# Performance work log

Measured on AMD Instinct MI355X. Metric: run time of the kernel, lower is better.

The kernel has to match this reference:

```python
import jax, jax.numpy as jnp
import numpy as np

B, V, N, IN_F, HEADS, OUT_F = 4, 4, 1000, 64, 4, 32
D = HEADS * OUT_F  # 128, concat=True
E = 64000
NEG_SLOPE = 0.2


def setup_inputs() -> dict:
    key = jax.random.key(0)
    ks = jax.random.split(key, 8)
    x = jax.random.normal(ks[0], (B, V, N, IN_F), jnp.float32)
    edge_index = jax.random.randint(ks[1], (2, E), 0, B * N, dtype=jnp.int64)
    W = jax.random.normal(ks[2], (HEADS * OUT_F, IN_F), jnp.float32) / np.sqrt(IN_F)
    att = jax.random.normal(ks[3], (1, HEADS, 2 * OUT_F), jnp.float32) * 0.1
    in_proj_w = jax.random.normal(ks[4], (3 * D, D), jnp.float32) / np.sqrt(D)
    in_proj_b = jnp.zeros((3 * D,), jnp.float32)
    out_proj_w = jax.random.normal(ks[5], (D, D), jnp.float32) / np.sqrt(D)
    out_proj_b = jnp.zeros((D,), jnp.float32)
    bias = jnp.zeros((D,), jnp.float32)
    return dict(x=x, W=W, att=att, in_proj_w=in_proj_w, in_proj_b=in_proj_b,
                out_proj_w=out_proj_w, out_proj_b=out_proj_b, bias=bias,
                edge_index=edge_index)


def reference(x, W, att, in_proj_w, in_proj_b, out_proj_w, out_proj_b, bias, edge_index):
    Bx, Vx, Nx, _ = x.shape
    Ntot = Bx * Nx
    # intra-view GAT: shared W across views
    h = jnp.einsum('bvni,oi->bvno', x, W).reshape(Bx, Vx, Nx, HEADS, OUT_F)
    # block-diagonal placement: h_full[b*V+v, b*N:(b+1)*N] = h[b,v]
    ib = jnp.arange(Bx)
    hf = jnp.zeros((Bx, Vx, Bx, Nx, HEADS, OUT_F), x.dtype).at[ib, :, ib].set(h)
    h_full = hf.reshape(Bx * Vx, Ntot, HEADS, OUT_F)
    # add self loops
    loops = jnp.arange(Ntot, dtype=edge_index.dtype)
    src = jnp.concatenate([edge_index[0], loops])
    dst = jnp.concatenate([edge_index[1], loops])
    # attention scores (faithful to source: flatten h_full over (B*V, Ntot) and
    # index with raw node ids, i.e. gathers from block 0 only)
    h_flat = h_full.reshape(Bx * Vx * Ntot, HEADS, OUT_F)
    h_cat = jnp.concatenate([h_flat[src], h_flat[dst]], axis=-1)  # [Etot, H, 2*OUT]
    att_in = jax.nn.leaky_relu(h_cat, NEG_SLOPE)
    scores = jnp.sum(att * att_in, axis=-1)  # [Etot, HEADS]
    # per-destination segment softmax
    seg_max = jax.ops.segment_max(scores, dst, num_segments=Ntot)
    seg_max = jax.lax.stop_gradient(jnp.where(jnp.isfinite(seg_max), seg_max, 0.0))
    ex = jnp.exp(scores - seg_max[dst])
    denom = jax.ops.segment_sum(ex, dst, num_segments=Ntot)
    alpha = ex / (denom[dst] + 1e-16)  # [Etot, HEADS]
    # scatter-add aggregation, broadcast over B*V rows
    msgs = h_full[:, src] * alpha[None, :, :, None]  # [B*V, Etot, H, OUT]
    out_full = jnp.zeros_like(h_full).at[:, dst].add(msgs)
    # extract each graph's own node block
    out = out_full.reshape(Bx, Vx, Bx, Nx, HEADS, OUT_F)[ib, :, ib]  # [B,V,N,H,OUT]
    h_gat = out.reshape(Bx, Vx, Nx, HEADS * OUT_F)  # concat heads
    # inter-view mixing: MHA over the V axis per node
    seq = h_gat.transpose(0, 2, 1, 3).reshape(Bx * Nx, Vx, D)
    q, k, v = jnp.split(seq @ in_proj_w.T + in_proj_b, 3, axis=-1)
    hd = D // HEADS
    sp = lambda t: t.reshape(Bx * Nx, Vx, HEADS, hd).transpose(0, 2, 1, 3)
    q, k, v = sp(q), sp(k), sp(v)
    aw = jax.nn.softmax(jnp.einsum('bhqd,bhkd->bhqk', q, k) / jnp.sqrt(jnp.asarray(hd, x.dtype)), axis=-1)
    ao = jnp.einsum('bhqk,bhkd->bhqd', aw, v).transpose(0, 2, 1, 3).reshape(Bx * Nx, Vx, D)
    mixed = ao @ out_proj_w.T + out_proj_b
    h_mixed = mixed.reshape(Bx, Nx, Vx, D).transpose(0, 2, 1, 3)  # [B,V,N,D]
    return h_mixed + bias
```

## Files before the change

kernel.cpp:

```cpp
#include <hip/hip_runtime.h>

#define NN 1000
#define HEADS_ 4
#define DM 128
#define EE 64000
#define NTOT 4000
#define ETOT 68000
#define CAP 48
#define EB 34

template <int K, int SCORE>
__device__ void gemm_tile(int mi, int ni,
                          const float* __restrict__ A, const float* __restrict__ Wt,
                          float* __restrict__ C, int N,
                          const float* __restrict__ att,
                          float* __restrict__ ssrc, float* __restrict__ sdst) {
  __shared__ float As[128 * 64];
  __shared__ float Bs[64 * 64];
  int tid = threadIdx.x;
  int m0 = mi * 128, n0 = ni * 64;
  int tx = tid & 15, ty = tid >> 4;
  const float4* A4 = (const float4*)A;
  const float4* W4 = (const float4*)Wt;
  float acc[8][4] = {};

  for (int c = 0; c < K / 64; ++c) {
    __syncthreads();
    {
      int q = tid & 15;
      int r0 = tid >> 4;
#pragma unroll
      for (int p = 0; p < 8; ++p) {
        int r = r0 + p * 16;
        float4 v = A4[(size_t)(m0 + r) * (K / 4) + c * 16 + q];
        *(float4*)&As[r * 64 + ((q ^ ((r >> 2) & 15)) << 2)] = v;
      }
#pragma unroll
      for (int p = 0; p < 4; ++p) {
        int r = r0 + p * 16;
        float4 v = W4[(size_t)(n0 + r) * (K / 4) + c * 16 + q];
        *(float4*)&Bs[r * 64 + ((q ^ ((r >> 2) & 15)) << 2)] = v;
      }
    }
    __syncthreads();
#pragma unroll 4
    for (int q = 0; q < 16; ++q) {
      float4 a[8], b[4];
#pragma unroll
      for (int i = 0; i < 8; ++i) {
        int r = ty * 8 + i;
        a[i] = *(const float4*)&As[r * 64 + ((q ^ ((r >> 2) & 15)) << 2)];
      }
#pragma unroll
      for (int j = 0; j < 4; ++j) {
        int rn = tx * 4 + j;
        b[j] = *(const float4*)&Bs[rn * 64 + ((q ^ ((rn >> 2) & 15)) << 2)];
      }
#pragma unroll
      for (int i = 0; i < 8; ++i)
#pragma unroll
        for (int j = 0; j < 4; ++j)
          acc[i][j] += a[i].x * b[j].x + a[i].y * b[j].y
                     + a[i].z * b[j].z + a[i].w * b[j].w;
    }
  }

  int nc = n0 + tx * 4;
#pragma unroll
  for (int i = 0; i < 8; ++i) {
    int m = m0 + ty * 8 + i;
    float4 o = make_float4(acc[i][0], acc[i][1], acc[i][2], acc[i][3]);
    *(float4*)&C[(size_t)m * N + nc] = o;
  }

  if (SCORE && m0 < NN) {
    int hsel = tx >> 3;
    int h = ni * 2 + hsel;
    int kb = (tx & 7) * 4;
    float a0[4], a1[4];
#pragma unroll
    for (int j = 0; j < 4; ++j) {
      a0[j] = att[h * 64 + kb + j];
      a1[j] = att[h * 64 + 32 + kb + j];
    }
#pragma unroll
    for (int i = 0; i < 8; ++i) {
      int m = m0 + ty * 8 + i;
      float p0 = 0.f, p1 = 0.f;
#pragma unroll
      for (int j = 0; j < 4; ++j) {
        float g = acc[i][j];
        float lr = g > 0.f ? g : 0.2f * g;
        p0 += a0[j] * lr;
        p1 += a1[j] * lr;
      }
      p0 += __shfl_xor(p0, 1, 16); p1 += __shfl_xor(p1, 1, 16);
      p0 += __shfl_xor(p0, 2, 16); p1 += __shfl_xor(p1, 2, 16);
      p0 += __shfl_xor(p0, 4, 16); p1 += __shfl_xor(p1, 4, 16);
      if ((tx & 7) == 0 && m < NN) {
        ssrc[m * HEADS_ + h] = p0;
        sdst[m * HEADS_ + h] = p1;
      }
    }
  }
}

__global__ __launch_bounds__(256) void k1_kernel(const float* __restrict__ x,
                                                 const float* __restrict__ W,
                                                 const float* __restrict__ att,
                                                 float* __restrict__ hbuf,
                                                 float* __restrict__ ssrc,
                                                 float* __restrict__ sdst,
                                                 const int* __restrict__ ei,
                                                 int* __restrict__ cnt,
                                                 int* __restrict__ elist) {
  int bid = blockIdx.x;
  if (bid < 250) {
    gemm_tile<64, 1>(bid >> 1, bid & 1, x, W, hbuf, 128, att, ssrc, sdst);
  } else {
    for (int e = (bid - 250) * 256 + threadIdx.x; e < ETOT; e += EB * 256) {
      int s, d;
      if (e < EE) { s = ei[e]; d = ei[EE + e]; }
      else { s = d = e - EE; }
      int pos = atomicAdd(&cnt[d], 1);
      if (pos < CAP) elist[d * CAP + pos] = s;
    }
  }
}

__global__ __launch_bounds__(256) void gather_kernel(const int* __restrict__ cnt,
                                                     const int* __restrict__ elist,
                                                     const float* __restrict__ ssrc,
                                                     const float* __restrict__ sdst,
                                                     const float* __restrict__ hbuf,
                                                     float* __restrict__ hgat) {
  __shared__ int   srcs[2][CAP];
  __shared__ float exs[2][CAP][HEADS_];
  int li = threadIdx.x >> 7;
  int t = threadIdx.x & 127;
  int d = blockIdx.x * 2 + li;
  int b = d / NN;
  int v = t >> 5, q = t & 31, h = q >> 3;
  int m = cnt[d]; if (m > CAP) m = CAP;
  for (int base = 0; base < m; base += 32) {
    int i = base + (t >> 2);
    if (i < m) {
      int s = elist[d * CAP + i];
      if ((t & 3) == 0) srcs[li][i] = s;
      float sc = ssrc[s * HEADS_ + (t & 3)] + sdst[d * HEADS_ + (t & 3)];
      exs[li][i][t & 3] = __expf(sc);
    }
  }
  __syncthreads();
  float den = 1e-16f;
  float4 acc = make_float4(0.f, 0.f, 0.f, 0.f);
  const float* hbase = hbuf + ((size_t)(b * 4 + v) * NN) * DM + q * 4;
  for (int i = 0; i < m; ++i) {
    float ex = exs[li][i][h];
    den += ex;
    unsigned sl = (unsigned)(srcs[li][i] - b * NN);
    if (sl < NN) {
      float4 hv = *(const float4*)(hbase + (size_t)sl * DM);
      acc.x += ex * hv.x; acc.y += ex * hv.y;
      acc.z += ex * hv.z; acc.w += ex * hv.w;
    }
  }
  float r = 1.f / den;
  acc.x *= r; acc.y *= r; acc.z *= r; acc.w *= r;
  *(float4*)&hgat[((size_t)(d * 4 + v)) * DM + q * 4] = acc;
}

#define QS 388

__global__ __launch_bounds__(512) void fused3_kernel(const float* __restrict__ hgat,
                                                     const float* __restrict__ inw,
                                                     const float* __restrict__ inb,
                                                     const float* __restrict__ outw,
                                                     const float* __restrict__ outb,
                                                     const float* __restrict__ bias,
                                                     float* __restrict__ out) {
  extern __shared__ float smem[];
  float* As = smem;
  float* Bs = smem + 4096;
  float* qk = smem + 12288;
  float* ao = qk;

  int tid = threadIdx.x;
  int g0 = blockIdx.x * 16;
  int tx = tid & 31, ty = tid >> 5;

  const float4* H4 = (const float4*)(hgat + (size_t)(g0 * 4) * DM);
  const float4* W4 = (const float4*)inw;

  float acc[3][4][4] = {};
#pragma unroll
  for (int c = 0; c < 2; ++c) {
#pragma unroll
    for (int ni = 0; ni < 3; ++ni) {
      __syncthreads();
      {
        int q = tid & 15, r0 = tid >> 4;
        if (ni == 0) {
#pragma unroll
          for (int p = 0; p < 2; ++p) {
            int r = r0 + p * 32;
            float4 v = H4[r * 32 + c * 16 + q];
            *(float4*)&As[r * 64 + ((q ^ ((r >> 2) & 15)) << 2)] = v;
          }
        }
#pragma unroll
        for (int p = 0; p < 4; ++p) {
          int r = r0 + p * 32;
          float4 v = W4[(size_t)(ni * 128 + r) * 32 + c * 16 + q];
          *(float4*)&Bs[r * 64 + ((q ^ ((r >> 2) & 15)) << 2)] = v;
        }
      }
      __syncthreads();
#pragma unroll 4
      for (int q = 0; q < 16; ++q) {
        float4 a[4], b[4];
        int sa = (q ^ ty) << 2;
        int sb = (q ^ (tx & 15)) << 2;
#pragma unroll
        for (int i = 0; i < 4; ++i)
          a[i] = *(const float4*)&As[(ty * 4 + i) * 64 + sa];
#pragma unroll
        for (int j = 0; j < 4; ++j)
          b[j] = *(const float4*)&Bs[(tx * 4 + j) * 64 + sb];
#pragma unroll
        for (int i = 0; i < 4; ++i)
#pragma unroll
          for (int j = 0; j < 4; ++j)
            acc[ni][i][j] += a[i].x * b[j].x + a[i].y * b[j].y
                           + a[i].z * b[j].z + a[i].w * b[j].w;
      }
    }
  }

#pragma unroll
  for (int ni = 0; ni < 3; ++ni) {
    int nc = ni * 128 + tx * 4;
    float4 bb = *(const float4*)&inb[nc];
#pragma unroll
    for (int i = 0; i < 4; ++i) {
      int r = ty * 4 + i;
      *(float4*)&qk[r * QS + nc] =
          make_float4(acc[ni][i][0] + bb.x, acc[ni][i][1] + bb.y,
                      acc[ni][i][2] + bb.z, acc[ni][i][3] + bb.w);
    }
  }
  __syncthreads();

  int ln = tid >> 5;
  int vq2 = (tid >> 3) & 3, h2 = (tid >> 1) & 3, s2 = tid & 1;
  float aww[4];
  {
    const float* qr = &qk[(ln * 4 + vq2) * QS + h2 * 32 + s2 * 16];
    float4 qv[4];
#pragma unroll
    for (int u = 0; u < 4; ++u) qv[u] = *(const float4*)&qr[u * 4];
    float sc[4];
#pragma unroll
    for (int vk = 0; vk < 4; ++vk) {
      const float* kr = &qk[(ln * 4 + vk) * QS + 128 + h2 * 32 + s2 * 16];
      float s = 0.f;
#pragma unroll
      for (int u = 0; u < 4; ++u) {
        float4 kv = *(const float4*)&kr[u * 4];
        s += qv[u].x * kv.x + qv[u].y * kv.y + qv[u].z * kv.z + qv[u].w * kv.w;
      }
      sc[vk] = s;
    }
#pragma unroll
    for (int vk = 0; vk < 4; ++vk)
      sc[vk] = (sc[vk] + __shfl_xor(sc[vk], 1)) * 0.17677669529663687f;
    float mx = fmaxf(fmaxf(sc[0], sc[1]), fmaxf(sc[2], sc[3]));
    float e0 = __expf(sc[0] - mx), e1 = __expf(sc[1] - mx);
    float e2 = __expf(sc[2] - mx), e3 = __expf(sc[3] - mx);
    float inv = 1.f / (e0 + e1 + e2 + e3);
    aww[0] = e0 * inv; aww[1] = e1 * inv; aww[2] = e2 * inv; aww[3] = e3 * inv;
  }

  float4 o[4];
#pragma unroll
  for (int u = 0; u < 4; ++u) o[u] = make_float4(0.f, 0.f, 0.f, 0.f);
#pragma unroll
  for (int vk = 0; vk < 4; ++vk) {
    const float* vr = &qk[(ln * 4 + vk) * QS + 256 + h2 * 32 + s2 * 16];
    float w = aww[vk];
#pragma unroll
    for (int u = 0; u < 4; ++u) {
      float4 vv = *(const float4*)&vr[u * 4];
      o[u].x += w * vv.x; o[u].y += w * vv.y;
      o[u].z += w * vv.z; o[u].w += w * vv.w;
    }
  }
  __syncthreads();
  {
    int r = ln * 4 + vq2;
#pragma unroll
    for (int u = 0; u < 4; ++u) {
      int qp = h2 * 8 + s2 * 4 + u;
      int cc = qp >> 4, qg = qp & 15;
      *(float4*)&ao[cc * 4096 + r * 64 + ((qg ^ (ln & 15)) << 2)] = o[u];
    }
  }
  __syncthreads();

  float oc[4][4] = {};
  const float4* O4 = (const float4*)outw;
#pragma unroll
  for (int c = 0; c < 2; ++c) {
    {
      int q = tid & 15, r0 = tid >> 4;
#pragma unroll
      for (int p = 0; p < 4; ++p) {
        int r = r0 + p * 32;
        float4 v = O4[(size_t)r * 32 + c * 16 + q];
        *(float4*)&Bs[r * 64 + ((q ^ ((r >> 2) & 15)) << 2)] = v;
      }
    }
    __syncthreads();
#pragma unroll 4
    for (int q = 0; q < 16; ++q) {
      float4 a[4], b[4];
      int sa = (q ^ ty) << 2;
      int sb = (q ^ (tx & 15)) << 2;
#pragma unroll
      for (int i = 0; i < 4; ++i)
        a[i] = *(const float4*)&ao[c * 4096 + (ty * 4 + i) * 64 + sa];
#pragma unroll
      for (int j = 0; j < 4; ++j)
        b[j] = *(const float4*)&Bs[(tx * 4 + j) * 64 + sb];
#pragma unroll
      for (int i = 0; i < 4; ++i)
#pragma unroll
        for (int j = 0; j < 4; ++j)
          oc[i][j] += a[i].x * b[j].x + a[i].y * b[j].y
                    + a[i].z * b[j].z + a[i].w * b[j].w;
    }
    __syncthreads();
  }

  {
    int nc = tx * 4;
    float4 ob = make_float4(outb[nc] + bias[nc], outb[nc + 1] + bias[nc + 1],
                            outb[nc + 2] + bias[nc + 2], outb[nc + 3] + bias[nc + 3]);
#pragma unroll
    for (int i = 0; i < 4; ++i) {
      int r = ty * 4 + i;
      int node = g0 + (r >> 2), v = r & 3;
      int bg = node / NN, n = node - bg * NN;
      int om = (bg * 4 + v) * NN + n;
      *(float4*)&out[(size_t)om * DM + nc] =
          make_float4(oc[i][0] + ob.x, oc[i][1] + ob.y,
                      oc[i][2] + ob.z, oc[i][3] + ob.w);
    }
  }
}

extern "C" void kernel_launch(void* const* d_in, const int* in_sizes, int n_in,
                              void* d_out, int out_size, void* d_ws, size_t ws_size,
                              hipStream_t stream) {
  const float* x    = (const float*)d_in[0];
  const float* W    = (const float*)d_in[1];
  const float* att  = (const float*)d_in[2];
  const float* inw  = (const float*)d_in[3];
  const float* inb  = (const float*)d_in[4];
  const float* outw = (const float*)d_in[5];
  const float* outb = (const float*)d_in[6];
  const float* bias = (const float*)d_in[7];
  const int*   ei   = (const int*)d_in[8];
  float* out = (float*)d_out;

  float* ws = (float*)d_ws;
  float* hbuf  = ws;
  float* hgat  = ws + 2100000;
  float* ssrc  = ws + 12500000;
  float* sdst  = ssrc + 16000;
  int*   cnt   = (int*)(sdst + 16000);
  int*   elist = cnt + 4000;

  static int lds_opt_in = 0;
  if (!lds_opt_in) {
    hipFuncSetAttribute((const void*)fused3_kernel,
                        hipFuncAttributeMaxDynamicSharedMemorySize, 160 * 1024);
    lds_opt_in = 1;
  }

  hipMemsetAsync(ssrc, 0, 36000 * sizeof(float), stream);

  k1_kernel<<<250 + EB, 256, 0, stream>>>(x, W, att, hbuf, ssrc, sdst, ei, cnt, elist);
  gather_kernel<<<NTOT / 2, 256, 0, stream>>>(cnt, elist, ssrc, sdst, hbuf, hgat);
  fused3_kernel<<<250, 512, 148480, stream>>>(hgat, inw, inb, outw, outb, bias, out);
}
```

Measured before the change: 144.4 us.

## Retile GEMM kernels, restructure inter-view MHA into registers, unroll gather loop

The node-feature GEMM in k1 drops from 128-row to 64-row tiles, doubling the block count from 250 to 500. The fused MHA kernel is rewritten so each thread keeps Q, K and V for one node's four views in registers. Scores and the softmax are reduced with cross-lane shuffles instead of a large LDS staging area, which removes the 148KB dynamic shared memory and lets the kernel run 500 blocks of 256 threads. The gather loop is unrolled by four so several row loads are in flight at once, at the cost of more register pressure and a conditional-select pattern.

```diff
diff --git a/kernel.cpp b/kernel.cpp
--- a/kernel.cpp
+++ b/kernel.cpp
@@ -8,102 +8,6 @@
 #define ETOT 68000
 #define CAP 48
 #define EB 34
-
-template <int K, int SCORE>
-__device__ void gemm_tile(int mi, int ni,
-                          const float* __restrict__ A, const float* __restrict__ Wt,
-                          float* __restrict__ C, int N,
-                          const float* __restrict__ att,
-                          float* __restrict__ ssrc, float* __restrict__ sdst) {
-  __shared__ float As[128 * 64];
-  __shared__ float Bs[64 * 64];
-  int tid = threadIdx.x;
-  int m0 = mi * 128, n0 = ni * 64;
-  int tx = tid & 15, ty = tid >> 4;
-  const float4* A4 = (const float4*)A;
-  const float4* W4 = (const float4*)Wt;
-  float acc[8][4] = {};
-
-  for (int c = 0; c < K / 64; ++c) {
-    __syncthreads();
-    {
-      int q = tid & 15;
-      int r0 = tid >> 4;
-#pragma unroll
-      for (int p = 0; p < 8; ++p) {
-        int r = r0 + p * 16;
-        float4 v = A4[(size_t)(m0 + r) * (K / 4) + c * 16 + q];
-        *(float4*)&As[r * 64 + ((q ^ ((r >> 2) & 15)) << 2)] = v;
-      }
-#pragma unroll
-      for (int p = 0; p < 4; ++p) {
-        int r = r0 + p * 16;
-        float4 v = W4[(size_t)(n0 + r) * (K / 4) + c * 16 + q];
-        *(float4*)&Bs[r * 64 + ((q ^ ((r >> 2) & 15)) << 2)] = v;
-      }
-    }
-    __syncthreads();
-#pragma unroll 4
-    for (int q = 0; q < 16; ++q) {
-      float4 a[8], b[4];
-#pragma unroll
-      for (int i = 0; i < 8; ++i) {
-        int r = ty * 8 + i;
-        a[i] = *(const float4*)&As[r * 64 + ((q ^ ((r >> 2) & 15)) << 2)];
-      }
-#pragma unroll
-      for (int j = 0; j < 4; ++j) {
-        int rn = tx * 4 + j;
-        b[j] = *(const float4*)&Bs[rn * 64 + ((q ^ ((rn >> 2) & 15)) << 2)];
-      }
-#pragma unroll
-      for (int i = 0; i < 8; ++i)
-#pragma unroll
-        for (int j = 0; j < 4; ++j)
-          acc[i][j] += a[i].x * b[j].x + a[i].y * b[j].y
-                     + a[i].z * b[j].z + a[i].w * b[j].w;
-    }
-  }
-
-  int nc = n0 + tx * 4;
-#pragma unroll
-  for (int i = 0; i < 8; ++i) {
-    int m = m0 + ty * 8 + i;
-    float4 o = make_float4(acc[i][0], acc[i][1], acc[i][2], acc[i][3]);
-    *(float4*)&C[(size_t)m * N + nc] = o;
-  }
-
-  if (SCORE && m0 < NN) {
-    int hsel = tx >> 3;
-    int h = ni * 2 + hsel;
-    int kb = (tx & 7) * 4;
-    float a0[4], a1[4];
-#pragma unroll
-    for (int j = 0; j < 4; ++j) {
-      a0[j] = att[h * 64 + kb + j];
-      a1[j] = att[h * 64 + 32 + kb + j];
-    }
-#pragma unroll
-    for (int i = 0; i < 8; ++i) {
-      int m = m0 + ty * 8 + i;
-      float p0 = 0.f, p1 = 0.f;
-#pragma unroll
-      for (int j = 0; j < 4; ++j) {
-        float g = acc[i][j];
-        float lr = g > 0.f ? g : 0.2f * g;
-        p0 += a0[j] * lr;
-        p1 += a1[j] * lr;
-      }
-      p0 += __shfl_xor(p0, 1, 16); p1 += __shfl_xor(p1, 1, 16);
-      p0 += __shfl_xor(p0, 2, 16); p1 += __shfl_xor(p1, 2, 16);
-      p0 += __shfl_xor(p0, 4, 16); p1 += __shfl_xor(p1, 4, 16);
-      if ((tx & 7) == 0 && m < NN) {
-        ssrc[m * HEADS_ + h] = p0;
-        sdst[m * HEADS_ + h] = p1;
-      }
-    }
-  }
-}
 
 __global__ __launch_bounds__(256) void k1_kernel(const float* __restrict__ x,
                                                  const float* __restrict__ W,
@@ -115,10 +19,92 @@
                                                  int* __restrict__ cnt,
                                                  int* __restrict__ elist) {
   int bid = blockIdx.x;
-  if (bid < 250) {
-    gemm_tile<64, 1>(bid >> 1, bid & 1, x, W, hbuf, 128, att, ssrc, sdst);
+  if (bid < 500) {
+    __shared__ float As[64 * 64];
+    __shared__ float Bs[64 * 64];
+    int tid = threadIdx.x;
+    int mi = bid >> 1, ni = bid & 1;
+    int m0 = mi * 64, n0 = ni * 64;
+    int tx = tid & 15, ty = tid >> 4;
+    const float4* A4 = (const float4*)x;
+    const float4* W4 = (const float4*)W;
+    float acc[4][4] = {};
+
+    {
+      int q = tid & 15, r0 = tid >> 4;
+#pragma unroll
+      for (int p = 0; p < 4; ++p) {
+        int r = r0 + p * 16;
+        float4 v = A4[(size_t)(m0 + r) * 16 + q];
+        *(float4*)&As[r * 64 + ((q ^ ((r >> 2) & 15)) << 2)] = v;
+      }
+#pragma unroll
+      for (int p = 0; p < 4; ++p) {
+        int r = r0 + p * 16;
+        float4 v = W4[(size_t)(n0 + r) * 16 + q];
+        *(float4*)&Bs[r * 64 + ((q ^ ((r >> 2) & 15)) << 2)] = v;
+      }
+    }
+    __syncthreads();
+#pragma unroll 4
+    for (int q = 0; q < 16; ++q) {
+      float4 a[4], b[4];
+      int sa = (q ^ ty) << 2;
+      int sb = (q ^ tx) << 2;
+#pragma unroll
+      for (int i = 0; i < 4; ++i)
+        a[i] = *(const float4*)&As[(ty * 4 + i) * 64 + sa];
+#pragma unroll
+      for (int j = 0; j < 4; ++j)
+        b[j] = *(const float4*)&Bs[(tx * 4 + j) * 64 + sb];
+#pragma unroll
+      for (int i = 0; i < 4; ++i)
+#pragma unroll
+        for (int j = 0; j < 4; ++j)
+          acc[i][j] += a[i].x * b[j].x + a[i].y * b[j].y
+                     + a[i].z * b[j].z + a[i].w * b[j].w;
+    }
+
+    int nc = n0 + tx * 4;
+#pragma unroll
+    for (int i = 0; i < 4; ++i) {
+      int m = m0 + ty * 4 + i;
+      *(float4*)&hbuf[(size_t)m * DM + nc] =
+          make_float4(acc[i][0], acc[i][1], acc[i][2], acc[i][3]);
+    }
+
+    if (m0 < NN) {
+      int hsel = tx >> 3;
+      int h = ni * 2 + hsel;
+      int kb = (tx & 7) * 4;
+      float a0[4], a1[4];
+#pragma unroll
+      for (int j = 0; j < 4; ++j) {
+        a0[j] = att[h * 64 + kb + j];
+        a1[j] = att[h * 64 + 32 + kb + j];
+      }
+#pragma unroll
+      for (int i = 0; i < 4; ++i) {
+        int m = m0 + ty * 4 + i;
+        float p0 = 0.f, p1 = 0.f;
+#pragma unroll
+        for (int j = 0; j < 4; ++j) {
+          float g = acc[i][j];
+          float lr = g > 0.f ? g : 0.2f * g;
+          p0 += a0[j] * lr;
+          p1 += a1[j] * lr;
+        }
+        p0 += __shfl_xor(p0, 1, 16); p1 += __shfl_xor(p1, 1, 16);
+        p0 += __shfl_xor(p0, 2, 16); p1 += __shfl_xor(p1, 2, 16);
+        p0 += __shfl_xor(p0, 4, 16); p1 += __shfl_xor(p1, 4, 16);
+        if ((tx & 7) == 0 && m < NN) {
+          ssrc[m * HEADS_ + h] = p0;
+          sdst[m * HEADS_ + h] = p1;
+        }
+      }
+    }
   } else {
-    for (int e = (bid - 250) * 256 + threadIdx.x; e < ETOT; e += EB * 256) {
+    for (int e = (bid - 500) * 256 + threadIdx.x; e < ETOT; e += EB * 256) {
       int s, d;
       if (e < EE) { s = ei[e]; d = ei[EE + e]; }
       else { s = d = e - EE; }
@@ -155,7 +141,25 @@
   float den = 1e-16f;
   float4 acc = make_float4(0.f, 0.f, 0.f, 0.f);
   const float* hbase = hbuf + ((size_t)(b * 4 + v) * NN) * DM + q * 4;
-  for (int i = 0; i < m; ++i) {
+  int i = 0;
+  for (; i + 4 <= m; i += 4) {
+    float ex[4]; unsigned sl[4]; float4 hv[4];
+#pragma unroll
+    for (int u = 0; u < 4; ++u) {
+      ex[u] = exs[li][i + u][h];
+      sl[u] = (unsigned)(srcs[li][i + u] - b * NN);
+      unsigned sls = sl[u] < NN ? sl[u] : 0u;
+      hv[u] = *(const float4*)(hbase + (size_t)sls * DM);
+    }
+#pragma unroll
+    for (int u = 0; u < 4; ++u) {
+      den += ex[u];
+      float w = sl[u] < NN ? ex[u] : 0.f;
+      acc.x += w * hv[u].x; acc.y += w * hv[u].y;
+      acc.z += w * hv[u].z; acc.w += w * hv[u].w;
+    }
+  }
+  for (; i < m; ++i) {
     float ex = exs[li][i][h];
     den += ex;
     unsigned sl = (unsigned)(srcs[li][i] - b * NN);
@@ -170,188 +174,171 @@
   *(float4*)&hgat[((size_t)(d * 4 + v)) * DM + q * 4] = acc;
 }
 
-#define QS 388
-
-__global__ __launch_bounds__(512) void fused3_kernel(const float* __restrict__ hgat,
+__global__ __launch_bounds__(256) void fused3_kernel(const float* __restrict__ hgat,
                                                      const float* __restrict__ inw,
                                                      const float* __restrict__ inb,
                                                      const float* __restrict__ outw,
                                                      const float* __restrict__ outb,
                                                      const float* __restrict__ bias,
                                                      float* __restrict__ out) {
-  extern __shared__ float smem[];
-  float* As = smem;
-  float* Bs = smem + 4096;
-  float* qk = smem + 12288;
-  float* ao = qk;
+  __shared__ float smem[13312];
+  float* Bs  = smem;
+  float* As  = smem + 12288;
+  float* aoS = smem + 4096;
+  float* Ws2 = smem;
 
   int tid = threadIdx.x;
-  int g0 = blockIdx.x * 16;
-  int tx = tid & 31, ty = tid >> 5;
-
-  const float4* H4 = (const float4*)(hgat + (size_t)(g0 * 4) * DM);
+  int rg = tid & 7;
+  int cg = tid >> 3;
+  int blk = blockIdx.x;
+  int r0 = blk * 32;
+
+  const float4* H4 = (const float4*)hgat;
   const float4* W4 = (const float4*)inw;
 
   float acc[3][4][4] = {};
-#pragma unroll
-  for (int c = 0; c < 2; ++c) {
-#pragma unroll
-    for (int ni = 0; ni < 3; ++ni) {
-      __syncthreads();
-      {
-        int q = tid & 15, r0 = tid >> 4;
-        if (ni == 0) {
-#pragma unroll
-          for (int p = 0; p < 2; ++p) {
-            int r = r0 + p * 32;
-            float4 v = H4[r * 32 + c * 16 + q];
-            *(float4*)&As[r * 64 + ((q ^ ((r >> 2) & 15)) << 2)] = v;
-          }
-        }
-#pragma unroll
-        for (int p = 0; p < 4; ++p) {
-          int r = r0 + p * 32;
-          float4 v = W4[(size_t)(ni * 128 + r) * 32 + c * 16 + q];
-          *(float4*)&Bs[r * 64 + ((q ^ ((r >> 2) & 15)) << 2)] = v;
-        }
-      }
-      __syncthreads();
-#pragma unroll 4
-      for (int q = 0; q < 16; ++q) {
-        float4 a[4], b[4];
-        int sa = (q ^ ty) << 2;
-        int sb = (q ^ (tx & 15)) << 2;
+
+#pragma unroll
+  for (int c = 0; c < 4; ++c) {
+    __syncthreads();
+    {
+      int r = tid >> 3, kg = tid & 7;
+      float4 vv = H4[(size_t)(r0 + r) * 32 + c * 8 + kg];
+      *(float4*)&As[r * 32 + ((kg ^ ((r >> 2) & 7)) << 2)] = vv;
+    }
+#pragma unroll
+    for (int tt = 0; tt < 12; ++tt) {
+      int idx = tt * 256 + tid;
+      int col = idx >> 3, kg = idx & 7;
+      float4 vv = W4[(size_t)col * 32 + c * 8 + kg];
+      *(float4*)&Bs[col * 32 + ((kg ^ ((col >> 2) & 7)) << 2)] = vv;
+    }
+    __syncthreads();
+#pragma unroll
+    for (int q = 0; q < 8; ++q) {
+      float4 a[4], bb[3][4];
+      int ga = (q ^ rg) << 2;
+      int gb = (q ^ (cg & 7)) << 2;
+#pragma unroll
+      for (int i = 0; i < 4; ++i)
+        a[i] = *(const float4*)&As[(rg * 4 + i) * 32 + ga];
+#pragma unroll
+      for (int p = 0; p < 3; ++p)
+#pragma unroll
+        for (int j = 0; j < 4; ++j)
+          bb[p][j] = *(const float4*)&Bs[(p * 128 + cg * 4 + j) * 32 + gb];
+#pragma unroll
+      for (int p = 0; p < 3; ++p)
 #pragma unroll
         for (int i = 0; i < 4; ++i)
-          a[i] = *(const float4*)&As[(ty * 4 + i) * 64 + sa];
-#pragma unroll
-        for (int j = 0; j < 4; ++j)
-          b[j] = *(const float4*)&Bs[(tx * 4 + j) * 64 + sb];
-#pragma unroll
-        for (int i = 0; i < 4; ++i)
 #pragma unroll
           for (int j = 0; j < 4; ++j)
-            acc[ni][i][j] += a[i].x * b[j].x + a[i].y * b[j].y
-                           + a[i].z * b[j].z + a[i].w * b[j].w;
-      }
-    }
-  }
-
-#pragma unroll
-  for (int ni = 0; ni < 3; ++ni) {
-    int nc = ni * 128 + tx * 4;
-    float4 bb = *(const float4*)&inb[nc];
+            acc[p][i][j] += a[i].x * bb[p][j].x + a[i].y * bb[p][j].y
+                          + a[i].z * bb[p][j].z + a[i].w * bb[p][j].w;
+    }
+  }
+
+  {
+    float4 ib0 = *(const float4*)&inb[cg * 4];
+    float4 ib1 = *(const float4*)&inb[128 + cg * 4];
+    float4 ib2 = *(const float4*)&inb[256 + cg * 4];
 #pragma unroll
     for (int i = 0; i < 4; ++i) {
-      int r = ty * 4 + i;
-      *(float4*)&qk[r * QS + nc] =
-          make_float4(acc[ni][i][0] + bb.x, acc[ni][i][1] + bb.y,
-                      acc[ni][i][2] + bb.z, acc[ni][i][3] + bb.w);
-    }
-  }
-  __syncthreads();
-
-  int ln = tid >> 5;
-  int vq2 = (tid >> 3) & 3, h2 = (tid >> 1) & 3, s2 = tid & 1;
-  float aww[4];
-  {
-    const float* qr = &qk[(ln * 4 + vq2) * QS + h2 * 32 + s2 * 16];
-    float4 qv[4];
-#pragma unroll
-    for (int u = 0; u < 4; ++u) qv[u] = *(const float4*)&qr[u * 4];
-    float sc[4];
+      acc[0][i][0] += ib0.x; acc[0][i][1] += ib0.y; acc[0][i][2] += ib0.z; acc[0][i][3] += ib0.w;
+      acc[1][i][0] += ib1.x; acc[1][i][1] += ib1.y; acc[1][i][2] += ib1.z; acc[1][i][3] += ib1.w;
+      acc[2][i][0] += ib2.x; acc[2][i][1] += ib2.y; acc[2][i][2] += ib2.z; acc[2][i][3] += ib2.w;
+    }
+  }
+
+  float S[4][4];
+#pragma unroll
+  for (int vq = 0; vq < 4; ++vq)
+#pragma unroll
+    for (int vk = 0; vk < 4; ++vk)
+      S[vq][vk] = acc[0][vq][0] * acc[1][vk][0] + acc[0][vq][1] * acc[1][vk][1]
+                + acc[0][vq][2] * acc[1][vk][2] + acc[0][vq][3] * acc[1][vk][3];
+#pragma unroll
+  for (int vq = 0; vq < 4; ++vq)
 #pragma unroll
     for (int vk = 0; vk < 4; ++vk) {
-      const float* kr = &qk[(ln * 4 + vk) * QS + 128 + h2 * 32 + s2 * 16];
-      float s = 0.f;
-#pragma unroll
-      for (int u = 0; u < 4; ++u) {
-        float4 kv = *(const float4*)&kr[u * 4];
-        s += qv[u].x * kv.x + qv[u].y * kv.y + qv[u].z * kv.z + qv[u].w * kv.w;
-      }
-      sc[vk] = s;
-    }
-#pragma unroll
-    for (int vk = 0; vk < 4; ++vk)
-      sc[vk] = (sc[vk] + __shfl_xor(sc[vk], 1)) * 0.17677669529663687f;
-    float mx = fmaxf(fmaxf(sc[0], sc[1]), fmaxf(sc[2], sc[3]));
-    float e0 = __expf(sc[0] - mx), e1 = __expf(sc[1] - mx);
-    float e2 = __expf(sc[2] - mx), e3 = __expf(sc[3] - mx);
+      float s = S[vq][vk];
+      s += __shfl_xor(s, 8);
+      s += __shfl_xor(s, 16);
+      s += __shfl_xor(s, 32);
+      S[vq][vk] = s * 0.17677669529663687f;
+    }
+#pragma unroll
+  for (int vq = 0; vq < 4; ++vq) {
+    float mx = fmaxf(fmaxf(S[vq][0], S[vq][1]), fmaxf(S[vq][2], S[vq][3]));
+    float e0 = __expf(S[vq][0] - mx), e1 = __expf(S[vq][1] - mx);
+    float e2 = __expf(S[vq][2] - mx), e3 = __expf(S[vq][3] - mx);
     float inv = 1.f / (e0 + e1 + e2 + e3);
-    aww[0] = e0 * inv; aww[1] = e1 * inv; aww[2] = e2 * inv; aww[3] = e3 * inv;
-  }
-
-  float4 o[4];
-#pragma unroll
-  for (int u = 0; u < 4; ++u) o[u] = make_float4(0.f, 0.f, 0.f, 0.f);
-#pragma unroll
-  for (int vk = 0; vk < 4; ++vk) {
-    const float* vr = &qk[(ln * 4 + vk) * QS + 256 + h2 * 32 + s2 * 16];
-    float w = aww[vk];
-#pragma unroll
-    for (int u = 0; u < 4; ++u) {
-      float4 vv = *(const float4*)&vr[u * 4];
-      o[u].x += w * vv.x; o[u].y += w * vv.y;
-      o[u].z += w * vv.z; o[u].w += w * vv.w;
-    }
-  }
+    S[vq][0] = e0 * inv; S[vq][1] = e1 * inv; S[vq][2] = e2 * inv; S[vq][3] = e3 * inv;
+  }
+  float ao_r[4][4];
+#pragma unroll
+  for (int vq = 0; vq < 4; ++vq)
+#pragma unroll
+    for (int j = 0; j < 4; ++j)
+      ao_r[vq][j] = S[vq][0] * acc[2][0][j] + S[vq][1] * acc[2][1][j]
+                  + S[vq][2] * acc[2][2][j] + S[vq][3] * acc[2][3][j];
+
   __syncthreads();
   {
-    int r = ln * 4 + vq2;
-#pragma unroll
-    for (int u = 0; u < 4; ++u) {
-      int qp = h2 * 8 + s2 * 4 + u;
-      int cc = qp >> 4, qg = qp & 15;
-      *(float4*)&ao[cc * 4096 + r * 64 + ((qg ^ (ln & 15)) << 2)] = o[u];
-    }
-  }
-  __syncthreads();
-
+    int kc = cg >> 3, d4 = cg & 7;
+#pragma unroll
+    for (int vq = 0; vq < 4; ++vq) {
+      int r = rg * 4 + vq;
+      *(float4*)&aoS[kc * 1024 + r * 32 + ((d4 ^ rg) << 2)] =
+          make_float4(ao_r[vq][0], ao_r[vq][1], ao_r[vq][2], ao_r[vq][3]);
+    }
+  }
+
+  int rg2 = tid & 7, og = tid >> 3;
   float oc[4][4] = {};
   const float4* O4 = (const float4*)outw;
 #pragma unroll
-  for (int c = 0; c < 2; ++c) {
+  for (int kc = 0; kc < 4; ++kc) {
+    __syncthreads();
     {
-      int q = tid & 15, r0 = tid >> 4;
-#pragma unroll
-      for (int p = 0; p < 4; ++p) {
-        int r = r0 + p * 32;
-        float4 v = O4[(size_t)r * 32 + c * 16 + q];
-        *(float4*)&Bs[r * 64 + ((q ^ ((r >> 2) & 15)) << 2)] = v;
-      }
-    }
-    __syncthreads();
-#pragma unroll 4
-    for (int q = 0; q < 16; ++q) {
-      float4 a[4], b[4];
-      int sa = (q ^ ty) << 2;
-      int sb = (q ^ (tx & 15)) << 2;
-#pragma unroll
-      for (int i = 0; i < 4; ++i)
-        a[i] = *(const float4*)&ao[c * 4096 + (ty * 4 + i) * 64 + sa];
+#pragma unroll
+      for (int tt = 0; tt < 4; ++tt) {
+        int idx = tt * 256 + tid;
+        int col = idx >> 3, kg = idx & 7;
+        float4 vv = O4[(size_t)col * 32 + kc * 8 + kg];
+        *(float4*)&Ws2[col * 32 + ((kg ^ ((col >> 2) & 7)) << 2)] = vv;
+      }
+    }
+    __syncthreads();
+#pragma unroll
+    for (int q = 0; q < 8; ++q) {
+      float4 a[4], bq[4];
+      int ga = (q ^ rg2) << 2;
+      int gb = (q ^ (og & 7)) << 2;
+#pragma unroll
+      for (int i = 0; i < 4; ++i)
+        a[i] = *(const float4*)&aoS[kc * 1024 + (rg2 * 4 + i) * 32 + ga];
 #pragma unroll
       for (int j = 0; j < 4; ++j)
-        b[j] = *(const float4*)&Bs[(tx * 4 + j) * 64 + sb];
+        bq[j] = *(const float4*)&Ws2[(og * 4 + j) * 32 + gb];
 #pragma unroll
       for (int i = 0; i < 4; ++i)
 #pragma unroll
         for (int j = 0; j < 4; ++j)
-          oc[i][j] += a[i].x * b[j].x + a[i].y * b[j].y
-                    + a[i].z * b[j].z + a[i].w * b[j].w;
-    }
-    __syncthreads();
+          oc[i][j] += a[i].x * bq[j].x + a[i].y * bq[j].y
+                    + a[i].z * bq[j].z + a[i].w * bq[j].w;
+    }
   }
 
   {
-    int nc = tx * 4;
+    int nc = og * 4;
     float4 ob = make_float4(outb[nc] + bias[nc], outb[nc + 1] + bias[nc + 1],
                             outb[nc + 2] + bias[nc + 2], outb[nc + 3] + bias[nc + 3]);
 #pragma unroll
     for (int i = 0; i < 4; ++i) {
-      int r = ty * 4 + i;
-      int node = g0 + (r >> 2), v = r & 3;
+      int node = blk * 8 + rg2, vv = i;
       int bg = node / NN, n = node - bg * NN;
-      int om = (bg * 4 + v) * NN + n;
+      int om = (bg * 4 + vv) * NN + n;
       *(float4*)&out[(size_t)om * DM + nc] =
           make_float4(oc[i][0] + ob.x, oc[i][1] + ob.y,
                       oc[i][2] + ob.z, oc[i][3] + ob.w);
@@ -381,16 +368,9 @@
   int*   cnt   = (int*)(sdst + 16000);
   int*   elist = cnt + 4000;
 
-  static int lds_opt_in = 0;
-  if (!lds_opt_in) {
-    hipFuncSetAttribute((const void*)fused3_kernel,
-                        hipFuncAttributeMaxDynamicSharedMemorySize, 160 * 1024);
-    lds_opt_in = 1;
-  }
-
   hipMemsetAsync(ssrc, 0, 36000 * sizeof(float), stream);
 
-  k1_kernel<<<250 + EB, 256, 0, stream>>>(x, W, att, hbuf, ssrc, sdst, ei, cnt, elist);
+  k1_kernel<<<500 + EB, 256, 0, stream>>>(x, W, att, hbuf, ssrc, sdst, ei, cnt, elist);
   gather_kernel<<<NTOT / 2, 256, 0, stream>>>(cnt, elist, ssrc, sdst, hbuf, hgat);
-  fused3_kernel<<<250, 512, 148480, stream>>>(hgat, inw, inb, outw, outb, bias, out);
+  fused3_kernel<<<500, 256, 0, stream>>>(hgat, inw, inb, outw, outb, bias, out);
 }
```

New measurement: 545.3 us. +277.6%, slower.
